# Kernel tuning notes

Hardware: AMD Instinct MI355X
Metric: run time of the kernel (lower is better)

Reference implementation:

```python
import math
import jax, jax.numpy as jnp
import numpy as np

BSZ, N_HEADS, N_KV_HEADS, SEQLEN, HEAD_DIM = 1, 32, 8, 2048, 128
DIM = N_HEADS * HEAD_DIM  # 4096
N_REP = N_HEADS // N_KV_HEADS  # 4
NEG = -1e9


def setup_inputs() -> dict:
    key = jax.random.key(0)
    kq, kk, kv = jax.random.split(key, 3)
    q = jax.random.normal(kq, (BSZ, N_HEADS, SEQLEN, HEAD_DIM), dtype=jnp.float32)
    k = jax.random.normal(kk, (BSZ, N_KV_HEADS, SEQLEN, HEAD_DIM), dtype=jnp.float32)
    v = jax.random.normal(kv, (BSZ, N_KV_HEADS, SEQLEN, HEAD_DIM), dtype=jnp.float32)
    # additive causal mask: 0 on/below diagonal, large negative above
    causal = jnp.tril(jnp.ones((SEQLEN, SEQLEN), dtype=bool))
    mask = jnp.where(causal, 0.0, NEG).astype(jnp.float32)
    input_pos = jnp.zeros((1,), dtype=jnp.int64)
    return {"input_pos": input_pos, "q": q, "k": k, "v": v,
            "bsz": BSZ, "seqlen": SEQLEN, "mask": mask}


def reference(input_pos, q, k, v, bsz, seqlen, mask):
    # repeat_kv: (b, n_kv, s, d) -> (b, n_kv*n_rep, s, d), repeat_interleave on head dim
    k = jnp.repeat(k, N_REP, axis=1)
    v = jnp.repeat(v, N_REP, axis=1)
    scale = 1.0 / math.sqrt(q.shape[-1])
    # (b, h, s, s)
    attn = jnp.einsum("bhqd,bhkd->bhqk", q, k) * scale + mask
    attn = jax.nn.softmax(attn, axis=-1)
    y = jnp.einsum("bhqk,bhkd->bhqd", attn, v)  # (b, h, s, d)
    return y.transpose(0, 2, 1, 3).reshape(bsz, seqlen, DIM)
```

## Files before the change

kernel.cpp:

```cpp
#include <hip/hip_runtime.h>
#include <hip/hip_bf16.h>

#define SEQ 2048
#define HD 128
#define NH 32
#define NKV 8
#define ODIM 4096
#define QB 64
#define KVB 64
#define SCALE 0.08838834764831845f
#define NEGBIG -1e9f

typedef __attribute__((ext_vector_type(8))) short bf16x8;
typedef __attribute__((ext_vector_type(4))) float f32x4;
typedef __attribute__((ext_vector_type(16))) float f32x16;
typedef __attribute__((ext_vector_type(2))) int i32x2;

__device__ __forceinline__ unsigned short f2bf(float x) {
  union { __hip_bfloat16 b; unsigned short u; } c;
  c.b = __float2bfloat16(x);
  return c.u;
}

__device__ __forceinline__ unsigned pack2bf(float lo, float hi) {
  union { __hip_bfloat162 h; unsigned u; } c;
  c.h = __float22bfloat162_rn(float2{lo, hi});
  return c.u;
}

__device__ __forceinline__ void gload_lds16(const unsigned char* g, unsigned char* l) {
  __builtin_amdgcn_global_load_lds(
      (const __attribute__((address_space(1))) void*)g,
      (__attribute__((address_space(3))) void*)l, 16, 0, 0);
}

#define KWORK (NKV * SEQ * 16)
#define VWORK (NKV * (SEQ / 2) * 16)
__global__ __launch_bounds__(256) void sdpa_prepass(
    const float* __restrict__ k, const float* __restrict__ v,
    unsigned char* __restrict__ ws) {
  unsigned char* kimg = ws;
  unsigned char* vimg = ws + (NKV * 32 * 16384);
  int idx = (int)blockIdx.x * 256 + (int)threadIdx.x;
  if (idx < KWORK) {
    int hkv = idx >> 15;
    int rem = idx & 32767;
    int rg = rem >> 4;
    int c8 = (rem & 15) << 3;
    const float* src = k + ((size_t)hkv * SEQ + rg) * HD + c8;
    float4 a = *(const float4*)(src);
    float4 b = *(const float4*)(src + 4);
    union { unsigned short hh[8]; uint4 u4; } pk;
    pk.hh[0]=f2bf(a.x); pk.hh[1]=f2bf(a.y); pk.hh[2]=f2bf(a.z); pk.hh[3]=f2bf(a.w);
    pk.hh[4]=f2bf(b.x); pk.hh[5]=f2bf(b.y); pk.hh[6]=f2bf(b.z); pk.hh[7]=f2bf(b.w);
    int t = rg >> 6, r = rg & 63;
    size_t base = ((size_t)(hkv * 32 + t)) << 14;
    *(uint4*)(kimg + base + (r << 8) + ((c8 << 1) ^ ((r & 7) << 4))) = pk.u4;
  } else {
    int u = idx - KWORK;
    if (u >= VWORK) return;
    int hkv = u >> 14;
    int rem = u & 16383;
    int pr = rem >> 4;
    int d0 = (rem & 15) << 3;
    int rg = pr << 1;
    const float* s0 = v + ((size_t)hkv * SEQ + rg) * HD + d0;
    const float* s1 = s0 + HD;
    float4 a0 = *(const float4*)(s0);
    float4 b0 = *(const float4*)(s0 + 4);
    float4 a1 = *(const float4*)(s1);
    float4 b1 = *(const float4*)(s1 + 4);
    float lo[8] = {a0.x,a0.y,a0.z,a0.w,b0.x,b0.y,b0.z,b0.w};
    float hi[8] = {a1.x,a1.y,a1.z,a1.w,b1.x,b1.y,b1.z,b1.w};
    int t = rg >> 6, rr = rg & 63;
    size_t base = ((size_t)(hkv * 32 + t)) << 14;
    int rb = rr << 1;
    #pragma unroll
    for (int j = 0; j < 8; ++j) {
      int d = d0 + j;
      *(unsigned*)(vimg + base + (d << 7) + (rb ^ ((d & 7) << 4))) =
          pack2bf(lo[j], hi[j]);
    }
  }
}

__global__ __launch_bounds__(256, 2) void sdpa_flash_kernel(
    const float* __restrict__ q, const unsigned char* __restrict__ kimg,
    const unsigned char* __restrict__ vimg, float* __restrict__ out) {
  __shared__ __align__(16) unsigned char smem[65536];
  const int tid = threadIdx.x;
  const int w = tid >> 6;
  const int l = tid & 63;
  const int q31 = l & 31;
  const int hi = l >> 5;

  const int p = (int)blockIdx.x;
  const int qtA = p, qtB = 31 - p;
  const int myqt = (w < 2) ? qtA : qtB;
  const int h = (int)blockIdx.y;
  const int hkv = h >> 2;
  const int qbase = myqt * QB + 32 * (w & 1);
  const int myq = qbase + q31;

  bf16x8 qa[8];
  {
    const float* qr = q + ((size_t)(h * SEQ + myq)) * HD + 8 * hi;
    #pragma unroll
    for (int s = 0; s < 8; ++s) {
      float4 a = *(const float4*)(qr + 16 * s);
      float4 b = *(const float4*)(qr + 16 * s + 4);
      union { unsigned short hh[8]; bf16x8 vv; } pk;
      pk.hh[0] = f2bf(a.x * SCALE); pk.hh[1] = f2bf(a.y * SCALE);
      pk.hh[2] = f2bf(a.z * SCALE); pk.hh[3] = f2bf(a.w * SCALE);
      pk.hh[4] = f2bf(b.x * SCALE); pk.hh[5] = f2bf(b.y * SCALE);
      pk.hh[6] = f2bf(b.z * SCALE); pk.hh[7] = f2bf(b.w * SCALE);
      qa[s] = pk.vv;
    }
  }

  f32x16 o[4];
  #pragma unroll
  for (int db = 0; db < 4; ++db)
    #pragma unroll
    for (int r = 0; r < 16; ++r) o[db][r] = 0.f;
  float mrow = -1e30f, lrow = 0.f;

  const int ntiles = qtB + 1;
  const unsigned char* kt0 = kimg + (((size_t)(hkv * 32)) << 14);
  const unsigned char* vt0 = vimg + (((size_t)(hkv * 32)) << 14);

#define STAGE(tt, bufbase) {                                   \
    const unsigned char* ks_ = kt0 + (((size_t)(tt)) << 14);   \
    const unsigned char* vs_ = vt0 + (((size_t)(tt)) << 14);   \
    unsigned char* Kb_ = (bufbase) + (w << 12);                \
    unsigned char* Vb_ = (bufbase) + 16384 + (w << 12);        \
    const unsigned char* kso_ = ks_ + (w << 12) + (l << 4);    \
    const unsigned char* vso_ = vs_ + (w << 12) + (l << 4);    \
    gload_lds16(kso_, Kb_);                                    \
    gload_lds16(kso_ + 1024, Kb_ + 1024);                      \
    gload_lds16(kso_ + 2048, Kb_ + 2048);                      \
    gload_lds16(kso_ + 3072, Kb_ + 3072);                      \
    gload_lds16(vso_, Vb_);                                    \
    gload_lds16(vso_ + 1024, Vb_ + 1024);                      \
    gload_lds16(vso_ + 2048, Vb_ + 2048);                      \
    gload_lds16(vso_ + 3072, Vb_ + 3072);                      \
  }

  STAGE(0, smem);
  __syncthreads();
  int cur = 0;

  for (int t = 0; t < ntiles; ++t) {
    const int kv0 = t * KVB;
    if (t + 1 < ntiles) STAGE(t + 1, smem + ((cur ^ 1) << 15));

    unsigned char* Klds = smem + (cur << 15);
    unsigned char* Vlds = Klds + 16384;

    if (t <= myqt) {
      f32x16 s0, s1;
      #pragma unroll
      for (int r = 0; r < 16; ++r) { s0[r] = 0.f; s1[r] = 0.f; }
      __builtin_amdgcn_s_setprio(1);
      #pragma unroll
      for (int s = 0; s < 8; ++s) {
        int colb = 32 * s + 16 * hi;
        int r0 = q31;
        bf16x8 k0 = *(const bf16x8*)(Klds + (r0 << 8) + (colb ^ ((r0 & 7) << 4)));
        int r1 = 32 + q31;
        bf16x8 k1 = *(const bf16x8*)(Klds + (r1 << 8) + (colb ^ ((r1 & 7) << 4)));
        s0 = __builtin_amdgcn_mfma_f32_32x32x16_bf16(k0, qa[s], s0, 0, 0, 0);
        s1 = __builtin_amdgcn_mfma_f32_32x32x16_bf16(k1, qa[s], s1, 0, 0, 0);
      }
      __builtin_amdgcn_s_setprio(0);

      if (t == myqt) {
        #pragma unroll
        for (int r = 0; r < 16; ++r) {
          int kvr = kv0 + (r & 3) + 8 * (r >> 2) + 4 * hi;
          s0[r] += (kvr > myq) ? NEGBIG : 0.f;
          s1[r] += (kvr + 32 > myq) ? NEGBIG : 0.f;
        }
      }

      float tm = -1e30f;
      #pragma unroll
      for (int r = 0; r < 16; ++r) {
        tm = fmaxf(tm, s0[r]);
        tm = fmaxf(tm, s1[r]);
      }
      tm = fmaxf(tm, __shfl_xor(tm, 32));
      float mn = fmaxf(mrow, tm);
      if (!__all(tm <= mrow + 8.0f)) {
        float fac = __expf(mrow - mn);
        mrow = mn;
        lrow *= fac;
        #pragma unroll
        for (int db = 0; db < 4; ++db)
          #pragma unroll
          for (int r = 0; r < 16; ++r) o[db][r] *= fac;
      }
      float rs = 0.f;
      #pragma unroll
      for (int r = 0; r < 16; ++r) {
        s0[r] = __expf(s0[r] - mrow); rs += s0[r];
        s1[r] = __expf(s1[r] - mrow); rs += s1[r];
      }
      rs += __shfl_xor(rs, 32);
      lrow += rs;

      bf16x8 pf[4];
      #pragma unroll
      for (int s2 = 0; s2 < 2; ++s2) {
        {
          unsigned a0 = pack2bf(s0[8*s2+0], s0[8*s2+1]);
          unsigned a1 = pack2bf(s0[8*s2+2], s0[8*s2+3]);
          unsigned b0 = pack2bf(s0[8*s2+4], s0[8*s2+5]);
          unsigned b1 = pack2bf(s0[8*s2+6], s0[8*s2+7]);
          i32x2 r0 = __builtin_amdgcn_permlane32_swap((int)a0, (int)b0, false, false);
          i32x2 r1 = __builtin_amdgcn_permlane32_swap((int)a1, (int)b1, false, false);
          union { int u[4]; bf16x8 v; } pw;
          pw.u[0] = r0.x; pw.u[1] = r1.x; pw.u[2] = r0.y; pw.u[3] = r1.y;
          pf[s2] = pw.v;
        }
        {
          unsigned a0 = pack2bf(s1[8*s2+0], s1[8*s2+1]);
          unsigned a1 = pack2bf(s1[8*s2+2], s1[8*s2+3]);
          unsigned b0 = pack2bf(s1[8*s2+4], s1[8*s2+5]);
          unsigned b1 = pack2bf(s1[8*s2+6], s1[8*s2+7]);
          i32x2 r0 = __builtin_amdgcn_permlane32_swap((int)a0, (int)b0, false, false);
          i32x2 r1 = __builtin_amdgcn_permlane32_swap((int)a1, (int)b1, false, false);
          union { int u[4]; bf16x8 v; } pw;
          pw.u[0] = r0.x; pw.u[1] = r1.x; pw.u[2] = r0.y; pw.u[3] = r1.y;
          pf[2 + s2] = pw.v;
        }
      }

      __builtin_amdgcn_s_setprio(1);
      #pragma unroll
      for (int s = 0; s < 4; ++s) {
        int colb = 32 * s + 16 * hi;
        #pragma unroll
        for (int db = 0; db < 4; ++db) {
          int dd = db * 32 + q31;
          bf16x8 vf = *(const bf16x8*)(Vlds + (dd << 7) + (colb ^ ((dd & 7) << 4)));
          o[db] = __builtin_amdgcn_mfma_f32_32x32x16_bf16(vf, pf[s], o[db], 0, 0, 0);
        }
      }
      __builtin_amdgcn_s_setprio(0);
    }

    __syncthreads();
    cur ^= 1;
  }

  float inv = 1.f / lrow;
  float* obase = out + (size_t)myq * ODIM + h * HD;
  #pragma unroll
  for (int db = 0; db < 4; ++db) {
    #pragma unroll
    for (int c = 0; c < 4; ++c) {
      int d0 = db * 32 + 8 * c + 4 * hi;
      float4 st = {o[db][4*c+0] * inv, o[db][4*c+1] * inv,
                   o[db][4*c+2] * inv, o[db][4*c+3] * inv};
      *(float4*)(obase + d0) = st;
    }
  }
#undef STAGE
}

__global__ __launch_bounds__(512, 4) void sdpa_flash_fb(
    const float* __restrict__ q, const float* __restrict__ k,
    const float* __restrict__ v, float* __restrict__ out) {
  __shared__ __align__(16) unsigned char smem[65536];
  const int tid = threadIdx.x;
  const int w = tid >> 6;
  const int l = tid & 63;
  const int lm = l & 15;
  const int lg = l >> 4;
  const int p = (int)blockIdx.x;
  const int qtA = p;
  const int qtB = 31 - p;
  const int myqt = (w < 4) ? qtA : qtB;
  const int h = (int)blockIdx.y;
  const int hkv = h >> 2;
  const int qbase = myqt * QB + 16 * (w & 3);
  const int myrow = qbase + lm;
  bf16x8 qa[4];
  {
    const float* qr = q + ((size_t)(h * SEQ + myrow)) * HD + 8 * lg;
    #pragma unroll
    for (int c = 0; c < 4; ++c) {
      float4 a = *(const float4*)(qr + 32 * c);
      float4 b = *(const float4*)(qr + 32 * c + 4);
      union { unsigned short hh[8]; bf16x8 vv; } pk;
      pk.hh[0] = f2bf(a.x * SCALE); pk.hh[1] = f2bf(a.y * SCALE);
      pk.hh[2] = f2bf(a.z * SCALE); pk.hh[3] = f2bf(a.w * SCALE);
      pk.hh[4] = f2bf(b.x * SCALE); pk.hh[5] = f2bf(b.y * SCALE);
      pk.hh[6] = f2bf(b.z * SCALE); pk.hh[7] = f2bf(b.w * SCALE);
      qa[c] = pk.vv;
    }
  }
  f32x4 o[8];
  #pragma unroll
  for (int i = 0; i < 8; ++i) o[i] = (f32x4){0.f, 0.f, 0.f, 0.f};
  float mrow = -1e30f;
  float lrow = 0.f;
  const int ntiles = qtB + 1;
  const float* kg0 = k + (size_t)hkv * SEQ * HD;
  const float* vg0 = v + (size_t)hkv * SEQ * HD;
  const int k_r0 = tid >> 4;
  const int k_c8 = (tid & 15) << 3;
  const int v_rr = (tid & 31) << 1;
  const int v_d0 = (tid >> 5) << 3;
  float4 ka0, kb0, ka1, kb1, va0, vb0, va1, vb1;
#define LOADT(tt) {                                                          \
    const float* kg_ = kg0 + (size_t)((tt) * KVB) * HD + k_r0 * HD + k_c8;   \
    ka0 = *(const float4*)(kg_);                                             \
    kb0 = *(const float4*)(kg_ + 4);                                         \
    ka1 = *(const float4*)(kg_ + 32 * HD);                                   \
    kb1 = *(const float4*)(kg_ + 32 * HD + 4);                               \
    const float* vg_ = vg0 + (size_t)((tt) * KVB) * HD + v_rr * HD + v_d0;   \
    va0 = *(const float4*)(vg_);                                             \
    vb0 = *(const float4*)(vg_ + 4);                                         \
    va1 = *(const float4*)(vg_ + HD);                                        \
    vb1 = *(const float4*)(vg_ + HD + 4);                                    \
  }
#define WRITELDS(bufbase) {                                                  \
    unsigned char* Kb_ = (bufbase);                                          \
    unsigned char* Vb_ = (bufbase) + 16384;                                  \
    {                                                                        \
      union { unsigned short hh[8]; uint4 u4; } pk_;                         \
      pk_.hh[0]=f2bf(ka0.x); pk_.hh[1]=f2bf(ka0.y);                          \
      pk_.hh[2]=f2bf(ka0.z); pk_.hh[3]=f2bf(ka0.w);                          \
      pk_.hh[4]=f2bf(kb0.x); pk_.hh[5]=f2bf(kb0.y);                          \
      pk_.hh[6]=f2bf(kb0.z); pk_.hh[7]=f2bf(kb0.w);                          \
      int byte_ = (k_r0 << 8) + ((k_c8 << 1) ^ ((k_r0 & 7) << 4));           \
      *(uint4*)(Kb_ + byte_) = pk_.u4;                                       \
    }                                                                        \
    {                                                                        \
      int r1_ = k_r0 + 32;                                                   \
      union { unsigned short hh[8]; uint4 u4; } pk_;                         \
      pk_.hh[0]=f2bf(ka1.x); pk_.hh[1]=f2bf(ka1.y);                          \
      pk_.hh[2]=f2bf(ka1.z); pk_.hh[3]=f2bf(ka1.w);                          \
      pk_.hh[4]=f2bf(kb1.x); pk_.hh[5]=f2bf(kb1.y);                          \
      pk_.hh[6]=f2bf(kb1.z); pk_.hh[7]=f2bf(kb1.w);                          \
      int byte_ = (r1_ << 8) + ((k_c8 << 1) ^ ((r1_ & 7) << 4));             \
      *(uint4*)(Kb_ + byte_) = pk_.u4;                                       \
    }                                                                        \
    {                                                                        \
      unsigned w0_ = pack2bf(va0.x, va1.x), w1_ = pack2bf(va0.y, va1.y);     \
      unsigned w2_ = pack2bf(va0.z, va1.z), w3_ = pack2bf(va0.w, va1.w);     \
      unsigned w4_ = pack2bf(vb0.x, vb1.x), w5_ = pack2bf(vb0.y, vb1.y);     \
      unsigned w6_ = pack2bf(vb0.z, vb1.z), w7_ = pack2bf(vb0.w, vb1.w);     \
      int rb_ = v_rr << 1;                                                   \
      int d_;                                                                \
      d_ = v_d0;     *(unsigned*)(Vb_ + (d_ << 7) + (rb_ ^ ((d_ & 7) << 4))) = w0_; \
      d_ = v_d0 + 1; *(unsigned*)(Vb_ + (d_ << 7) + (rb_ ^ ((d_ & 7) << 4))) = w1_; \
      d_ = v_d0 + 2; *(unsigned*)(Vb_ + (d_ << 7) + (rb_ ^ ((d_ & 7) << 4))) = w2_; \
      d_ = v_d0 + 3; *(unsigned*)(Vb_ + (d_ << 7) + (rb_ ^ ((d_ & 7) << 4))) = w3_; \
      d_ = v_d0 + 4; *(unsigned*)(Vb_ + (d_ << 7) + (rb_ ^ ((d_ & 7) << 4))) = w4_; \
      d_ = v_d0 + 5; *(unsigned*)(Vb_ + (d_ << 7) + (rb_ ^ ((d_ & 7) << 4))) = w5_; \
      d_ = v_d0 + 6; *(unsigned*)(Vb_ + (d_ << 7) + (rb_ ^ ((d_ & 7) << 4))) = w6_; \
      d_ = v_d0 + 7; *(unsigned*)(Vb_ + (d_ << 7) + (rb_ ^ ((d_ & 7) << 4))) = w7_; \
    }                                                                        \
  }
  LOADT(0);
  WRITELDS(smem);
  __syncthreads();
  int cur = 0;
  for (int t = 0; t < ntiles; ++t) {
    const int kv0 = t * KVB;
    const bool have_next = (t + 1 < ntiles);
    if (have_next) LOADT(t + 1);
    unsigned char* Klds = smem + (cur << 15);
    unsigned char* Vlds = Klds + 16384;
    if (t <= myqt) {
      f32x4 s[4];
      #pragma unroll
      for (int nt = 0; nt < 4; ++nt) s[nt] = (f32x4){0.f, 0.f, 0.f, 0.f};
      #pragma unroll
      for (int nt = 0; nt < 4; ++nt) {
        int r = (nt << 4) + lm;
        #pragma unroll
        for (int kc = 0; kc < 4; ++kc) {
          int byte = (r << 8) + (((kc << 6) + (lg << 4)) ^ ((r & 7) << 4));
          bf16x8 kb = *(const bf16x8*)(Klds + byte);
          s[nt] = __builtin_amdgcn_mfma_f32_16x16x32_bf16(kb, qa[kc], s[nt], 0, 0, 0);
        }
      }
      if (kv0 + KVB - 1 > qbase) {
        #pragma unroll
        for (int nt = 0; nt < 4; ++nt) {
          #pragma unroll
          for (int i = 0; i < 4; ++i) {
            int col = kv0 + (nt << 4) + (lg << 2) + i;
            s[nt][i] += (col > myrow) ? NEGBIG : 0.f;
          }
        }
      }
      float tm = -1e30f;
      #pragma unroll
      for (int nt = 0; nt < 4; ++nt)
        #pragma unroll
        for (int i = 0; i < 4; ++i) tm = fmaxf(tm, s[nt][i]);
      tm = fmaxf(tm, __shfl_xor(tm, 16));
      tm = fmaxf(tm, __shfl_xor(tm, 32));
      float mn = fmaxf(mrow, tm);
      float fac = __expf(mrow - mn);
      mrow = mn;
      float rs = 0.f;
      #pragma unroll
      for (int nt = 0; nt < 4; ++nt) {
        #pragma unroll
        for (int i = 0; i < 4; ++i) {
          float pv = __expf(s[nt][i] - mn);
          s[nt][i] = pv;
          rs += pv;
        }
      }
      rs += __shfl_xor(rs, 16);
      rs += __shfl_xor(rs, 32);
      lrow = lrow * fac + rs;
      #pragma unroll
      for (int nt2 = 0; nt2 < 8; ++nt2) {
        #pragma unroll
        for (int i = 0; i < 4; ++i) o[nt2][i] *= fac;
      }
      unsigned pk0[4], pk1[4];
      #pragma unroll
      for (int nt = 0; nt < 4; ++nt) {
        pk0[nt] = pack2bf(s[nt][0], s[nt][1]);
        pk1[nt] = pack2bf(s[nt][2], s[nt][3]);
      }
      const int srcA = lm + ((lg & 1) << 5);
      const int srcB = srcA + 16;
      const bool lo2 = (lg < 2);
      bf16x8 pb[2];
      #pragma unroll
      for (int kc = 0; kc < 2; ++kc) {
        int a0 = __shfl((int)pk0[2*kc], srcA), b0 = __shfl((int)pk0[2*kc+1], srcA);
        int a1 = __shfl((int)pk1[2*kc], srcA), b1 = __shfl((int)pk1[2*kc+1], srcA);
        int a2 = __shfl((int)pk0[2*kc], srcB), b2 = __shfl((int)pk0[2*kc+1], srcB);
        int a3 = __shfl((int)pk1[2*kc], srcB), b3 = __shfl((int)pk1[2*kc+1], srcB);
        union { int uu[4]; bf16x8 v; } pw;
        pw.uu[0] = lo2 ? a0 : b0;
        pw.uu[1] = lo2 ? a1 : b1;
        pw.uu[2] = lo2 ? a2 : b2;
        pw.uu[3] = lo2 ? a3 : b3;
        pb[kc] = pw.v;
      }
      #pragma unroll
      for (int nt2 = 0; nt2 < 8; ++nt2) {
        int dr = (nt2 << 4) + lm;
        #pragma unroll
        for (int kc = 0; kc < 2; ++kc) {
          int byte = (dr << 7) + (((kc << 6) + (lg << 4)) ^ ((dr & 7) << 4));
          bf16x8 vb = *(const bf16x8*)(Vlds + byte);
          o[nt2] = __builtin_amdgcn_mfma_f32_16x16x32_bf16(vb, pb[kc], o[nt2], 0, 0, 0);
        }
      }
    }
    if (have_next) {
      WRITELDS(smem + ((cur ^ 1) << 15));
    }
    __syncthreads();
    cur ^= 1;
  }
  float inv = 1.f / lrow;
  float* orow = out + (size_t)myrow * ODIM + h * HD + (lg << 2);
  #pragma unroll
  for (int nt2 = 0; nt2 < 8; ++nt2) {
    float4 st = {o[nt2][0] * inv, o[nt2][1] * inv, o[nt2][2] * inv, o[nt2][3] * inv};
    *(float4*)(orow + (nt2 << 4)) = st;
  }
#undef LOADT
#undef WRITELDS
}

extern "C" void kernel_launch(void* const* d_in, const int* in_sizes, int n_in,
                              void* d_out, int out_size, void* d_ws, size_t ws_size,
                              hipStream_t stream) {
  const float* q = (const float*)d_in[1];
  const float* k = (const float*)d_in[2];
  const float* v = (const float*)d_in[3];
  float* out = (float*)d_out;
  dim3 grid(SEQ / QB / 2, NH);
  const size_t need = (size_t)(NKV * 32 * 16384) * 2;
  if (ws_size >= need && d_ws != nullptr) {
    unsigned char* ws = (unsigned char*)d_ws;
    int total = KWORK + VWORK;
    sdpa_prepass<<<(total + 255) / 256, 256, 0, stream>>>(k, v, ws);
    sdpa_flash_kernel<<<grid, 256, 0, stream>>>(
        q, ws, ws + (NKV * 32 * 16384), out);
  } else {
    sdpa_flash_fb<<<grid, 512, 0, stream>>>(q, k, v, out);
  }
}
```

Baseline: 91.90 us.

## Split each KV tile across two waves per query strip and merge partial softmax

The block grows from 4 to 8 waves. Each pair of waves shares a 32-row query strip and processes half of every 64-row KV tile, each keeping its own running max, sum and output accumulator. At the end the two partial states are merged through shared memory using a log-sum-exp rescale before the output is written. This halves the per-wave MFMA and softmax work per tile and adds more waves for latency hiding. In exchange it costs an extra LDS round-trip and barrier at the end, duplicated Q registers per wave, and more shared memory per block, which may reduce occupancy.

```diff
diff --git a/kernel.cpp b/kernel.cpp
--- a/kernel.cpp
+++ b/kernel.cpp
@@ -84,22 +84,24 @@
   }
 }
 
-__global__ __launch_bounds__(256, 2) void sdpa_flash_kernel(
+__global__ __launch_bounds__(512, 4) void sdpa_flash_kernel(
     const float* __restrict__ q, const unsigned char* __restrict__ kimg,
     const unsigned char* __restrict__ vimg, float* __restrict__ out) {
-  __shared__ __align__(16) unsigned char smem[65536];
+  __shared__ __align__(16) unsigned char smem[67584];
   const int tid = threadIdx.x;
   const int w = tid >> 6;
   const int l = tid & 63;
   const int q31 = l & 31;
   const int hi = l >> 5;
+  const int kvh = w & 1;
+  const int strip = w >> 1;
 
   const int p = (int)blockIdx.x;
   const int qtA = p, qtB = 31 - p;
-  const int myqt = (w < 2) ? qtA : qtB;
+  const int myqt = (strip < 2) ? qtA : qtB;
   const int h = (int)blockIdx.y;
   const int hkv = h >> 2;
-  const int qbase = myqt * QB + 32 * (w & 1);
+  const int qbase = myqt * QB + 32 * (strip & 1);
   const int myq = qbase + q31;
 
   bf16x8 qa[8];
@@ -129,21 +131,15 @@
   const unsigned char* kt0 = kimg + (((size_t)(hkv * 32)) << 14);
   const unsigned char* vt0 = vimg + (((size_t)(hkv * 32)) << 14);
 
-#define STAGE(tt, bufbase) {                                   \
-    const unsigned char* ks_ = kt0 + (((size_t)(tt)) << 14);   \
-    const unsigned char* vs_ = vt0 + (((size_t)(tt)) << 14);   \
-    unsigned char* Kb_ = (bufbase) + (w << 12);                \
-    unsigned char* Vb_ = (bufbase) + 16384 + (w << 12);        \
-    const unsigned char* kso_ = ks_ + (w << 12) + (l << 4);    \
-    const unsigned char* vso_ = vs_ + (w << 12) + (l << 4);    \
-    gload_lds16(kso_, Kb_);                                    \
-    gload_lds16(kso_ + 1024, Kb_ + 1024);                      \
-    gload_lds16(kso_ + 2048, Kb_ + 2048);                      \
-    gload_lds16(kso_ + 3072, Kb_ + 3072);                      \
-    gload_lds16(vso_, Vb_);                                    \
-    gload_lds16(vso_ + 1024, Vb_ + 1024);                      \
-    gload_lds16(vso_ + 2048, Vb_ + 2048);                      \
-    gload_lds16(vso_ + 3072, Vb_ + 3072);                      \
+#define STAGE(tt, bufbase) {                                                  \
+    const unsigned char* ks_ = kt0 + (((size_t)(tt)) << 14) + (w << 11) + (l << 4); \
+    const unsigned char* vs_ = vt0 + (((size_t)(tt)) << 14) + (w << 11) + (l << 4); \
+    unsigned char* Kb_ = (bufbase) + (w << 11);                               \
+    unsigned char* Vb_ = (bufbase) + 16384 + (w << 11);                       \
+    gload_lds16(ks_, Kb_);                                                    \
+    gload_lds16(ks_ + 1024, Kb_ + 1024);                                      \
+    gload_lds16(vs_, Vb_);                                                    \
+    gload_lds16(vs_ + 1024, Vb_ + 1024);                                      \
   }
 
   STAGE(0, smem);
@@ -158,40 +154,33 @@
     unsigned char* Vlds = Klds + 16384;
 
     if (t <= myqt) {
-      f32x16 s0, s1;
-      #pragma unroll
-      for (int r = 0; r < 16; ++r) { s0[r] = 0.f; s1[r] = 0.f; }
+      f32x16 sa;
+      #pragma unroll
+      for (int r = 0; r < 16; ++r) sa[r] = 0.f;
+      const int kr = 32 * kvh + q31;
       __builtin_amdgcn_s_setprio(1);
       #pragma unroll
       for (int s = 0; s < 8; ++s) {
         int colb = 32 * s + 16 * hi;
-        int r0 = q31;
-        bf16x8 k0 = *(const bf16x8*)(Klds + (r0 << 8) + (colb ^ ((r0 & 7) << 4)));
-        int r1 = 32 + q31;
-        bf16x8 k1 = *(const bf16x8*)(Klds + (r1 << 8) + (colb ^ ((r1 & 7) << 4)));
-        s0 = __builtin_amdgcn_mfma_f32_32x32x16_bf16(k0, qa[s], s0, 0, 0, 0);
-        s1 = __builtin_amdgcn_mfma_f32_32x32x16_bf16(k1, qa[s], s1, 0, 0, 0);
+        bf16x8 kf = *(const bf16x8*)(Klds + (kr << 8) + (colb ^ ((kr & 7) << 4)));
+        sa = __builtin_amdgcn_mfma_f32_32x32x16_bf16(kf, qa[s], sa, 0, 0, 0);
       }
       __builtin_amdgcn_s_setprio(0);
 
       if (t == myqt) {
         #pragma unroll
         for (int r = 0; r < 16; ++r) {
-          int kvr = kv0 + (r & 3) + 8 * (r >> 2) + 4 * hi;
-          s0[r] += (kvr > myq) ? NEGBIG : 0.f;
-          s1[r] += (kvr + 32 > myq) ? NEGBIG : 0.f;
+          int kvr = kv0 + 32 * kvh + (r & 3) + 8 * (r >> 2) + 4 * hi;
+          sa[r] += (kvr > myq) ? NEGBIG : 0.f;
         }
       }
 
       float tm = -1e30f;
       #pragma unroll
-      for (int r = 0; r < 16; ++r) {
-        tm = fmaxf(tm, s0[r]);
-        tm = fmaxf(tm, s1[r]);
-      }
+      for (int r = 0; r < 16; ++r) tm = fmaxf(tm, sa[r]);
       tm = fmaxf(tm, __shfl_xor(tm, 32));
-      float mn = fmaxf(mrow, tm);
       if (!__all(tm <= mrow + 8.0f)) {
+        float mn = fmaxf(mrow, tm);
         float fac = __expf(mrow - mn);
         mrow = mn;
         lrow *= fac;
@@ -203,43 +192,40 @@
       float rs = 0.f;
       #pragma unroll
       for (int r = 0; r < 16; ++r) {
-        s0[r] = __expf(s0[r] - mrow); rs += s0[r];
-        s1[r] = __expf(s1[r] - mrow); rs += s1[r];
+        sa[r] = __expf(sa[r] - mrow);
+        rs += sa[r];
       }
       rs += __shfl_xor(rs, 32);
       lrow += rs;
 
-      bf16x8 pf[4];
-      #pragma unroll
-      for (int s2 = 0; s2 < 2; ++s2) {
-        {
-          unsigned a0 = pack2bf(s0[8*s2+0], s0[8*s2+1]);
-          unsigned a1 = pack2bf(s0[8*s2+2], s0[8*s2+3]);
-          unsigned b0 = pack2bf(s0[8*s2+4], s0[8*s2+5]);
-          unsigned b1 = pack2bf(s0[8*s2+6], s0[8*s2+7]);
-          i32x2 r0 = __builtin_amdgcn_permlane32_swap((int)a0, (int)b0, false, false);
-          i32x2 r1 = __builtin_amdgcn_permlane32_swap((int)a1, (int)b1, false, false);
-          union { int u[4]; bf16x8 v; } pw;
-          pw.u[0] = r0.x; pw.u[1] = r1.x; pw.u[2] = r0.y; pw.u[3] = r1.y;
-          pf[s2] = pw.v;
-        }
-        {
-          unsigned a0 = pack2bf(s1[8*s2+0], s1[8*s2+1]);
-          unsigned a1 = pack2bf(s1[8*s2+2], s1[8*s2+3]);
-          unsigned b0 = pack2bf(s1[8*s2+4], s1[8*s2+5]);
-          unsigned b1 = pack2bf(s1[8*s2+6], s1[8*s2+7]);
-          i32x2 r0 = __builtin_amdgcn_permlane32_swap((int)a0, (int)b0, false, false);
-          i32x2 r1 = __builtin_amdgcn_permlane32_swap((int)a1, (int)b1, false, false);
-          union { int u[4]; bf16x8 v; } pw;
-          pw.u[0] = r0.x; pw.u[1] = r1.x; pw.u[2] = r0.y; pw.u[3] = r1.y;
-          pf[2 + s2] = pw.v;
-        }
+      bf16x8 pf[2];
+      {
+        unsigned a0 = pack2bf(sa[0], sa[1]);
+        unsigned a1 = pack2bf(sa[2], sa[3]);
+        unsigned b0 = pack2bf(sa[4], sa[5]);
+        unsigned b1 = pack2bf(sa[6], sa[7]);
+        i32x2 r0 = __builtin_amdgcn_permlane32_swap((int)a0, (int)b0, false, false);
+        i32x2 r1 = __builtin_amdgcn_permlane32_swap((int)a1, (int)b1, false, false);
+        union { int u[4]; bf16x8 v; } pw;
+        pw.u[0] = r0.x; pw.u[1] = r1.x; pw.u[2] = r0.y; pw.u[3] = r1.y;
+        pf[0] = pw.v;
+      }
+      {
+        unsigned a0 = pack2bf(sa[8], sa[9]);
+        unsigned a1 = pack2bf(sa[10], sa[11]);
+        unsigned b0 = pack2bf(sa[12], sa[13]);
+        unsigned b1 = pack2bf(sa[14], sa[15]);
+        i32x2 r0 = __builtin_amdgcn_permlane32_swap((int)a0, (int)b0, false, false);
+        i32x2 r1 = __builtin_amdgcn_permlane32_swap((int)a1, (int)b1, false, false);
+        union { int u[4]; bf16x8 v; } pw;
+        pw.u[0] = r0.x; pw.u[1] = r1.x; pw.u[2] = r0.y; pw.u[3] = r1.y;
+        pf[1] = pw.v;
       }
 
       __builtin_amdgcn_s_setprio(1);
       #pragma unroll
-      for (int s = 0; s < 4; ++s) {
-        int colb = 32 * s + 16 * hi;
+      for (int s = 0; s < 2; ++s) {
+        int colb = 64 * kvh + 32 * s + 16 * hi;
         #pragma unroll
         for (int db = 0; db < 4; ++db) {
           int dd = db * 32 + q31;
@@ -254,16 +240,41 @@
     cur ^= 1;
   }
 
-  float inv = 1.f / lrow;
-  float* obase = out + (size_t)myq * ODIM + h * HD;
-  #pragma unroll
-  for (int db = 0; db < 4; ++db) {
+  unsigned char* Obuf = smem + strip * 16384;
+  float* mlbuf = (float*)(smem + 65536) + strip * 128;
+  if (kvh == 1) {
     #pragma unroll
-    for (int c = 0; c < 4; ++c) {
-      int d0 = db * 32 + 8 * c + 4 * hi;
-      float4 st = {o[db][4*c+0] * inv, o[db][4*c+1] * inv,
-                   o[db][4*c+2] * inv, o[db][4*c+3] * inv};
-      *(float4*)(obase + d0) = st;
+    for (int db = 0; db < 4; ++db) {
+      #pragma unroll
+      for (int c = 0; c < 4; ++c) {
+        float4 st = {o[db][4*c+0], o[db][4*c+1], o[db][4*c+2], o[db][4*c+3]};
+        *(float4*)(Obuf + ((db * 4 + c) << 10) + (l << 4)) = st;
+      }
+    }
+    mlbuf[l * 2] = mrow;
+    mlbuf[l * 2 + 1] = lrow;
+  }
+  __syncthreads();
+  if (kvh == 0) {
+    float m1 = mlbuf[l * 2];
+    float l1 = mlbuf[l * 2 + 1];
+    float m = fmaxf(mrow, m1);
+    float f0 = __expf(mrow - m);
+    float f1 = __expf(m1 - m);
+    float inv = 1.f / (lrow * f0 + l1 * f1);
+    float* obase = out + (size_t)myq * ODIM + h * HD;
+    #pragma unroll
+    for (int db = 0; db < 4; ++db) {
+      #pragma unroll
+      for (int c = 0; c < 4; ++c) {
+        float4 o1 = *(const float4*)(Obuf + ((db * 4 + c) << 10) + (l << 4));
+        int d0 = db * 32 + 8 * c + 4 * hi;
+        float4 st = {(o[db][4*c+0] * f0 + o1.x * f1) * inv,
+                     (o[db][4*c+1] * f0 + o1.y * f1) * inv,
+                     (o[db][4*c+2] * f0 + o1.z * f1) * inv,
+                     (o[db][4*c+3] * f0 + o1.w * f1) * inv};
+        *(float4*)(obase + d0) = st;
+      }
     }
   }
 #undef STAGE
@@ -491,7 +502,7 @@
     unsigned char* ws = (unsigned char*)d_ws;
     int total = KWORK + VWORK;
     sdpa_prepass<<<(total + 255) / 256, 256, 0, stream>>>(k, v, ws);
-    sdpa_flash_kernel<<<grid, 256, 0, stream>>>(
+    sdpa_flash_kernel<<<grid, 512, 0, stream>>>(
         q, ws, ws + (NKV * 32 * 16384), out);
   } else {
     sdpa_flash_fb<<<grid, 512, 0, stream>>>(q, k, v, out);
```

Measured after the change: 114.6 us. 1.25x slower.

## Use three rotating LDS buffers with split K/V staging and exp2-based softmax

Applied to the files above, without the earlier changes.

Replaces double-buffered K+V tiles (64KB LDS) with three 16KB buffers rotated per iteration. The next K tile loads during QK^T and the next V tile loads into the freed K buffer after a mid-iteration barrier. This cuts LDS use to 48KB, which may allow more blocks per CU, at the cost of an extra __syncthreads per tile. It also folds log2(e) into the Q scale so softmax uses the native exp2 instead of __expf, rescaling the mask constant and lazy-rescale threshold to match.

```diff
diff --git a/kernel.cpp b/kernel.cpp
--- a/kernel.cpp
+++ b/kernel.cpp
@@ -9,7 +9,10 @@
 #define QB 64
 #define KVB 64
 #define SCALE 0.08838834764831845f
+#define SCALE_L2E 0.12752767f
 #define NEGBIG -1e9f
+#define NEGBIG_L2 -1.4426950e9f
+#define THR_L2 11.54f
 
 typedef __attribute__((ext_vector_type(8))) short bf16x8;
 typedef __attribute__((ext_vector_type(4))) float f32x4;
@@ -87,7 +90,7 @@
 __global__ __launch_bounds__(256, 2) void sdpa_flash_kernel(
     const float* __restrict__ q, const unsigned char* __restrict__ kimg,
     const unsigned char* __restrict__ vimg, float* __restrict__ out) {
-  __shared__ __align__(16) unsigned char smem[65536];
+  __shared__ __align__(16) unsigned char smem[49152];
   const int tid = threadIdx.x;
   const int w = tid >> 6;
   const int l = tid & 63;
@@ -110,10 +113,10 @@
       float4 a = *(const float4*)(qr + 16 * s);
       float4 b = *(const float4*)(qr + 16 * s + 4);
       union { unsigned short hh[8]; bf16x8 vv; } pk;
-      pk.hh[0] = f2bf(a.x * SCALE); pk.hh[1] = f2bf(a.y * SCALE);
-      pk.hh[2] = f2bf(a.z * SCALE); pk.hh[3] = f2bf(a.w * SCALE);
-      pk.hh[4] = f2bf(b.x * SCALE); pk.hh[5] = f2bf(b.y * SCALE);
-      pk.hh[6] = f2bf(b.z * SCALE); pk.hh[7] = f2bf(b.w * SCALE);
+      pk.hh[0] = f2bf(a.x * SCALE_L2E); pk.hh[1] = f2bf(a.y * SCALE_L2E);
+      pk.hh[2] = f2bf(a.z * SCALE_L2E); pk.hh[3] = f2bf(a.w * SCALE_L2E);
+      pk.hh[4] = f2bf(b.x * SCALE_L2E); pk.hh[5] = f2bf(b.y * SCALE_L2E);
+      pk.hh[6] = f2bf(b.z * SCALE_L2E); pk.hh[7] = f2bf(b.w * SCALE_L2E);
       qa[s] = pk.vv;
     }
   }
@@ -128,36 +131,41 @@
   const int ntiles = qtB + 1;
   const unsigned char* kt0 = kimg + (((size_t)(hkv * 32)) << 14);
   const unsigned char* vt0 = vimg + (((size_t)(hkv * 32)) << 14);
-
-#define STAGE(tt, bufbase) {                                   \
-    const unsigned char* ks_ = kt0 + (((size_t)(tt)) << 14);   \
-    const unsigned char* vs_ = vt0 + (((size_t)(tt)) << 14);   \
-    unsigned char* Kb_ = (bufbase) + (w << 12);                \
-    unsigned char* Vb_ = (bufbase) + 16384 + (w << 12);        \
-    const unsigned char* kso_ = ks_ + (w << 12) + (l << 4);    \
-    const unsigned char* vso_ = vs_ + (w << 12) + (l << 4);    \
-    gload_lds16(kso_, Kb_);                                    \
-    gload_lds16(kso_ + 1024, Kb_ + 1024);                      \
-    gload_lds16(kso_ + 2048, Kb_ + 2048);                      \
-    gload_lds16(kso_ + 3072, Kb_ + 3072);                      \
-    gload_lds16(vso_, Vb_);                                    \
-    gload_lds16(vso_ + 1024, Vb_ + 1024);                      \
-    gload_lds16(vso_ + 2048, Vb_ + 2048);                      \
-    gload_lds16(vso_ + 3072, Vb_ + 3072);                      \
-  }
-
-  STAGE(0, smem);
+  const int woff = w << 12;
+
+#define STAGE_K(tt, Kb) {                                                    \
+    const unsigned char* ks_ = kt0 + (((size_t)(tt)) << 14) + woff + (l << 4); \
+    unsigned char* kd_ = (Kb) + woff;                                        \
+    gload_lds16(ks_, kd_);                                                   \
+    gload_lds16(ks_ + 1024, kd_ + 1024);                                     \
+    gload_lds16(ks_ + 2048, kd_ + 2048);                                     \
+    gload_lds16(ks_ + 3072, kd_ + 3072);                                     \
+  }
+#define STAGE_V(tt, Vb) {                                                    \
+    const unsigned char* vs_ = vt0 + (((size_t)(tt)) << 14) + woff + (l << 4); \
+    unsigned char* vd_ = (Vb) + woff;                                        \
+    gload_lds16(vs_, vd_);                                                   \
+    gload_lds16(vs_ + 1024, vd_ + 1024);                                     \
+    gload_lds16(vs_ + 2048, vd_ + 2048);                                     \
+    gload_lds16(vs_ + 3072, vd_ + 3072);                                     \
+  }
+
+  unsigned char* sA = smem;
+  unsigned char* sB = smem + 16384;
+  unsigned char* sC = smem + 32768;
+
+  STAGE_K(0, sA);
+  STAGE_V(0, sB);
   __syncthreads();
-  int cur = 0;
 
   for (int t = 0; t < ntiles; ++t) {
     const int kv0 = t * KVB;
-    if (t + 1 < ntiles) STAGE(t + 1, smem + ((cur ^ 1) << 15));
-
-    unsigned char* Klds = smem + (cur << 15);
-    unsigned char* Vlds = Klds + 16384;
-
-    if (t <= myqt) {
+    const bool have_next = (t + 1 < ntiles);
+    if (have_next) STAGE_K(t + 1, sC);
+
+    const bool act = (t <= myqt);
+    bf16x8 pf[4];
+    if (act) {
       f32x16 s0, s1;
       #pragma unroll
       for (int r = 0; r < 16; ++r) { s0[r] = 0.f; s1[r] = 0.f; }
@@ -166,9 +174,9 @@
       for (int s = 0; s < 8; ++s) {
         int colb = 32 * s + 16 * hi;
         int r0 = q31;
-        bf16x8 k0 = *(const bf16x8*)(Klds + (r0 << 8) + (colb ^ ((r0 & 7) << 4)));
+        bf16x8 k0 = *(const bf16x8*)(sA + (r0 << 8) + (colb ^ ((r0 & 7) << 4)));
         int r1 = 32 + q31;
-        bf16x8 k1 = *(const bf16x8*)(Klds + (r1 << 8) + (colb ^ ((r1 & 7) << 4)));
+        bf16x8 k1 = *(const bf16x8*)(sA + (r1 << 8) + (colb ^ ((r1 & 7) << 4)));
         s0 = __builtin_amdgcn_mfma_f32_32x32x16_bf16(k0, qa[s], s0, 0, 0, 0);
         s1 = __builtin_amdgcn_mfma_f32_32x32x16_bf16(k1, qa[s], s1, 0, 0, 0);
       }
@@ -178,8 +186,8 @@
         #pragma unroll
         for (int r = 0; r < 16; ++r) {
           int kvr = kv0 + (r & 3) + 8 * (r >> 2) + 4 * hi;
-          s0[r] += (kvr > myq) ? NEGBIG : 0.f;
-          s1[r] += (kvr + 32 > myq) ? NEGBIG : 0.f;
+          s0[r] += (kvr > myq) ? NEGBIG_L2 : 0.f;
+          s1[r] += (kvr + 32 > myq) ? NEGBIG_L2 : 0.f;
         }
       }
 
@@ -190,9 +198,9 @@
         tm = fmaxf(tm, s1[r]);
       }
       tm = fmaxf(tm, __shfl_xor(tm, 32));
-      float mn = fmaxf(mrow, tm);
-      if (!__all(tm <= mrow + 8.0f)) {
-        float fac = __expf(mrow - mn);
+      if (!__all(tm <= mrow + THR_L2)) {
+        float mn = fmaxf(mrow, tm);
+        float fac = __builtin_amdgcn_exp2f(mrow - mn);
         mrow = mn;
         lrow *= fac;
         #pragma unroll
@@ -203,13 +211,12 @@
       float rs = 0.f;
       #pragma unroll
       for (int r = 0; r < 16; ++r) {
-        s0[r] = __expf(s0[r] - mrow); rs += s0[r];
-        s1[r] = __expf(s1[r] - mrow); rs += s1[r];
+        s0[r] = __builtin_amdgcn_exp2f(s0[r] - mrow); rs += s0[r];
+        s1[r] = __builtin_amdgcn_exp2f(s1[r] - mrow); rs += s1[r];
       }
       rs += __shfl_xor(rs, 32);
       lrow += rs;
 
-      bf16x8 pf[4];
       #pragma unroll
       for (int s2 = 0; s2 < 2; ++s2) {
         {
@@ -235,7 +242,12 @@
           pf[2 + s2] = pw.v;
         }
       }
-
+    }
+
+    __syncthreads();
+    if (have_next) STAGE_V(t + 1, sA);
+
+    if (act) {
       __builtin_amdgcn_s_setprio(1);
       #pragma unroll
       for (int s = 0; s < 4; ++s) {
@@ -243,7 +255,7 @@
         #pragma unroll
         for (int db = 0; db < 4; ++db) {
           int dd = db * 32 + q31;
-          bf16x8 vf = *(const bf16x8*)(Vlds + (dd << 7) + (colb ^ ((dd & 7) << 4)));
+          bf16x8 vf = *(const bf16x8*)(sB + (dd << 7) + (colb ^ ((dd & 7) << 4)));
           o[db] = __builtin_amdgcn_mfma_f32_32x32x16_bf16(vf, pf[s], o[db], 0, 0, 0);
         }
       }
@@ -251,7 +263,10 @@
     }
 
     __syncthreads();
-    cur ^= 1;
+    unsigned char* nA = sC;
+    unsigned char* nB = sA;
+    unsigned char* nC = sB;
+    sA = nA; sB = nB; sC = nC;
   }
 
   float inv = 1.f / lrow;
@@ -266,7 +281,8 @@
       *(float4*)(obase + d0) = st;
     }
   }
-#undef STAGE
+#undef STAGE_K
+#undef STAGE_V
 }
 
 __global__ __launch_bounds__(512, 4) void sdpa_flash_fb(
@@ -485,15 +501,16 @@
   const float* k = (const float*)d_in[2];
   const float* v = (const float*)d_in[3];
   float* out = (float*)d_out;
-  dim3 grid(SEQ / QB / 2, NH);
   const size_t need = (size_t)(NKV * 32 * 16384) * 2;
   if (ws_size >= need && d_ws != nullptr) {
     unsigned char* ws = (unsigned char*)d_ws;
     int total = KWORK + VWORK;
     sdpa_prepass<<<(total + 255) / 256, 256, 0, stream>>>(k, v, ws);
+    dim3 grid(SEQ / QB / 2, NH);
     sdpa_flash_kernel<<<grid, 256, 0, stream>>>(
         q, ws, ws + (NKV * 32 * 16384), out);
   } else {
-    sdpa_flash_fb<<<grid, 512, 0, stream>>>(q, k, v, out);
-  }
-}
+    dim3 gridf(SEQ / QB / 2, NH);
+    sdpa_flash_fb<<<gridf, 512, 0, stream>>>(q, k, v, out);
+  }
+}
```

New measurement: 88.74 us. -3.4%, faster.
